# Performance work log

Measured on AMD Instinct MI355X. Metric: run time of the kernel, lower is better.

The kernel has to match this reference:

```python
import jax, jax.numpy as jnp
import numpy as np

B, INP, OUP, HID, H, W = 16, 32, 64, 192, 96, 96


def _relu6(t):
    return jnp.clip(t, 0.0, 6.0)


def _bn(t, g, b, m, v):
    # eval-mode BatchNorm2d, eps = 1e-5
    scale = g / jnp.sqrt(v + 1e-5)
    return (t - m[None, :, None, None]) * scale[None, :, None, None] + b[None, :, None, None]


def _up_bilinear_ac(img, Ho, Wo):
    # bilinear upsample with align_corners=True (torch upsample_bilinear)
    hin, win = img.shape[-2], img.shape[-1]
    def mk(nin, nout):
        c = jnp.arange(nout, dtype=jnp.float32) * ((nin - 1) / (nout - 1))
        i0 = jnp.clip(jnp.floor(c).astype(jnp.int32), 0, nin - 2)
        return i0, c - i0.astype(jnp.float32)
    r0, fr = mk(hin, Ho)
    c0, fc = mk(win, Wo)
    rows = img[..., r0, :] * (1.0 - fr)[:, None] + img[..., r0 + 1, :] * fr[:, None]
    return rows[..., c0] * (1.0 - fc) + rows[..., c0 + 1] * fc


def setup_inputs() -> dict:
    key = jax.random.key(0)
    ks = jax.random.split(key, 6)
    rn = lambda k, s, sc: jax.random.normal(k, s, dtype=jnp.float32) * sc
    return {
        'x': rn(ks[0], (B, INP, H, W), 1.0),
        'w1': rn(ks[1], (HID, INP), 0.1),
        'g1': jnp.ones((HID,), jnp.float32), 'b1': jnp.zeros((HID,), jnp.float32),
        'm1': jnp.zeros((HID,), jnp.float32), 'v1': jnp.ones((HID,), jnp.float32),
        'se_w': rn(ks[2], (1, HID), 0.1), 'se_b': jnp.zeros((1,), jnp.float32),
        'w_dw': rn(ks[3], (HID, 1, 3, 3), 0.1),
        'g2': jnp.ones((HID,), jnp.float32), 'b2': jnp.zeros((HID,), jnp.float32),
        'm2': jnp.zeros((HID,), jnp.float32), 'v2': jnp.ones((HID,), jnp.float32),
        'w2': rn(ks[4], (OUP, HID), 0.1),
        'g3': jnp.ones((OUP,), jnp.float32), 'b3': jnp.zeros((OUP,), jnp.float32),
        'm3': jnp.zeros((OUP,), jnp.float32), 'v3': jnp.ones((OUP,), jnp.float32),
    }


def reference(x, w1, g1, b1, m1, v1, se_w, se_b, w_dw, g2, b2, m2, v2, w2, g3, b3, m3, v3):
    tal = jnp.take_along_axis
    # expand 1x1 conv + BN + ReLU6
    y = jnp.einsum('bihw,oi->bohw', x, w1)
    y = _relu6(_bn(y, g1, b1, m1, v1))
    Bn, C, Hh, Ww = y.shape
    # SE branch: adaptive avg pool to 6x6 (H,W divisible by 6 -> uniform bins)
    yp = y.reshape(Bn, C, 6, Hh // 6, 6, Ww // 6).mean(axis=(3, 5))
    se = jnp.einsum('bchw,oc->bohw', yp, se_w) + se_b[None, :, None, None]
    se = jax.nn.sigmoid(se)
    se = _up_bilinear_ac(se, Hh, Ww)            # [B,1,H,W]
    y = y * se
    ys = se[:, 0]                                # [B,H,W]
    tc, tr = Ww // 2, Hh // 2
    # ---- row pass: content-adaptive sample positions via cumsum ----
    rm = ys + 0.001
    xx = jnp.cumsum((Ww * 0.5) / jnp.sum(rm, -1, keepdims=True) * rm + 0.5, axis=-1)
    xx = jax.lax.stop_gradient(xx)               # positions are detached
    cq = jnp.arange(tc, dtype=jnp.float32) * 2.0
    # searchsorted-left minus 1, clamped (torchinterp1d semantics)
    i = jnp.clip(jnp.sum(xx[..., None] < cq, axis=-2).astype(jnp.int32) - 1, 0, Ww - 2)  # [B,H,tc]
    x0 = tal(xx, i, -1); x1 = tal(xx, i + 1, -1)
    t = (cq - x0) / (x1 - x0)                    # [B,H,tc]
    ib = jnp.broadcast_to(i[:, None], (Bn, C, Hh, tc))
    y0 = tal(y, ib, -1); y1 = tal(y, ib + 1, -1)
    mf = y0 + (y1 - y0) * t[:, None]             # [B,C,H,tc]
    m0 = tal(ys, i, -1); m1_ = tal(ys, i + 1, -1)
    mm = m0 + (m1_ - m0) * t                     # [B,H,tc]
    # ---- column pass ----
    cm = mm + 0.001
    yy = jnp.cumsum((Hh * 0.5) / jnp.sum(cm, 1, keepdims=True) * cm + 0.5, axis=1)
    yy = jax.lax.stop_gradient(yy)               # [B,H,tc]
    yyT = jnp.swapaxes(yy, 1, 2)                 # [B,tc,H]
    rq = jnp.arange(tr, dtype=jnp.float32) * 2.0
    i2 = jnp.clip(jnp.sum(yyT[..., None] < rq, axis=-2).astype(jnp.int32) - 1, 0, Hh - 2)  # [B,tc,tr]
    p0 = tal(yyT, i2, -1); p1 = tal(yyT, i2 + 1, -1)
    t2 = (rq - p0) / (p1 - p0)                   # [B,tc,tr]
    mfT = jnp.swapaxes(mf, 2, 3)                 # [B,C,tc,H]
    i2b = jnp.broadcast_to(i2[:, None], (Bn, C, tc, tr))
    f0 = tal(mfT, i2b, -1); f1 = tal(mfT, i2b + 1, -1)
    ff = jnp.swapaxes(f0 + (f1 - f0) * t2[:, None], 2, 3)  # [B,C,tr,tc]
    # ---- tail: depthwise 3x3 + BN + ReLU6, project 1x1 + BN ----
    z = jax.lax.conv_general_dilated(ff, w_dw, (1, 1), 'SAME',
                                     feature_group_count=C,
                                     dimension_numbers=('NCHW', 'OIHW', 'NCHW'))
    z = _relu6(_bn(z, g2, b2, m2, v2))
    z = jnp.einsum('bchw,oc->bohw', z, w2)
    z = _bn(z, g3, b3, m3, v3)
    return z
```

## Files before the change

### kernel.cpp

```cpp
#include <hip/hip_runtime.h>
#include <hip/hip_bf16.h>
#include <math.h>

#define B_   16
#define INP  32
#define OUP  64
#define HID  192
#define H_   96
#define W_   96
#define HW_  (H_*W_)
#define TC   48
#define TR   48

typedef __attribute__((ext_vector_type(8))) short  bf16x8;
typedef __attribute__((ext_vector_type(4))) float  f32x4;

__device__ __forceinline__ float relu6f(float v) { return fminf(fmaxf(v, 0.f), 6.f); }
__device__ __forceinline__ float bf2f(unsigned short u) {
    unsigned int x = ((unsigned int)u) << 16;
    return __uint_as_float(x);
}
__device__ __forceinline__ unsigned short f2bf(float f) {
    unsigned int x = __float_as_uint(f);
    unsigned int lsb = (x >> 16) & 1u;
    x += 0x7fffu + lsb;
    return (unsigned short)(x >> 16);
}

__global__ __launch_bounds__(256) void k0_prep(
    const float* __restrict__ w1, const float* __restrict__ g1,
    const float* __restrict__ b1, const float* __restrict__ m1,
    const float* __restrict__ v1,
    const float* __restrict__ w2, const float* __restrict__ g3,
    const float* __restrict__ b3, const float* __restrict__ m3,
    const float* __restrict__ v3,
    unsigned short* __restrict__ w1b, float* __restrict__ t1,
    float* __restrict__ w2t, float* __restrict__ t3,
    float* __restrict__ se_part)
{
    const int idx = blockIdx.x*256 + threadIdx.x;
    if (idx < HID*INP) {
        int o = idx / INP;
        w1b[idx] = f2bf(w1[idx] * g1[o]*rsqrtf(v1[o] + 1e-5f));
    } else if (idx < HID*INP + HID) {
        int o = idx - HID*INP;
        float sc = g1[o]*rsqrtf(v1[o] + 1e-5f);
        t1[o] = b1[o] - m1[o]*sc;
    } else if (idx < HID*INP + HID + HID*OUP) {
        int k = idx - (HID*INP + HID);
        int c = k / OUP, o = k % OUP;
        w2t[k] = w2[o*HID + c] * g3[o]*rsqrtf(v3[o] + 1e-5f);
    } else if (idx < HID*INP + HID + HID*OUP + OUP) {
        int o = idx - (HID*INP + HID + HID*OUP);
        float sc = g3[o]*rsqrtf(v3[o] + 1e-5f);
        t3[o] = b3[o] - m3[o]*sc;
    } else if (idx < HID*INP + HID + HID*OUP + OUP + B_*36) {
        se_part[idx - (HID*INP + HID + HID*OUP + OUP)] = 0.f;
    }
}

__global__ __launch_bounds__(256) void k1_mfma(
    const float* __restrict__ x, const unsigned short* __restrict__ w1b,
    const float* __restrict__ t1, const float* __restrict__ se_w,
    unsigned short* __restrict__ y, float* __restrict__ se_part)
{
    __shared__ unsigned short wl[HID*INP];
    __shared__ unsigned short xT[64*INP];
    __shared__ float t1l[HID], sewl[HID];
    const int tid = threadIdx.x;
    const int bid = blockIdx.x;
    const int b   = bid / 144;
    const int inpx0 = (bid % 144) * 64;

    {
        const uint4* src = (const uint4*)w1b;
        uint4* dst = (uint4*)wl;
        dst[tid] = src[tid];
        if (tid < 256) { dst[tid+256] = src[tid+256]; dst[tid+512] = src[tid+512]; }
    }
    if (tid < HID) { t1l[tid] = t1[tid]; sewl[tid] = se_w[tid]; }
    {
        const int ch = tid >> 3, q8 = tid & 7;
        const float* xp = x + (size_t)(b*INP + ch)*HW_ + inpx0 + q8*8;
        float4 v0 = *(const float4*)(xp);
        float4 v1 = *(const float4*)(xp + 4);
        int p0 = q8*8;
        xT[(p0+0)*INP + ch] = f2bf(v0.x);
        xT[(p0+1)*INP + ch] = f2bf(v0.y);
        xT[(p0+2)*INP + ch] = f2bf(v0.z);
        xT[(p0+3)*INP + ch] = f2bf(v0.w);
        xT[(p0+4)*INP + ch] = f2bf(v1.x);
        xT[(p0+5)*INP + ch] = f2bf(v1.y);
        xT[(p0+6)*INP + ch] = f2bf(v1.z);
        xT[(p0+7)*INP + ch] = f2bf(v1.w);
    }
    __syncthreads();

    const int w = tid >> 6;
    const int l = tid & 63;
    const int pxl = l & 15;
    const int kb  = l >> 4;

    const bf16x8 bfrag = *(const bf16x8*)&xT[(w*16 + pxl)*INP + kb*8];

    const size_t ybase = (size_t)b*HID*HW_ + inpx0 + w*16 + pxl;
    float psum = 0.f;

    #pragma unroll
    for (int T = 0; T < 12; ++T) {
        const bf16x8 afrag = *(const bf16x8*)&wl[(T*16 + pxl)*INP + kb*8];
        f32x4 acc = __builtin_amdgcn_mfma_f32_16x16x32_bf16(
                        afrag, bfrag, (f32x4){0.f,0.f,0.f,0.f}, 0, 0, 0);
        const int oc0 = T*16 + kb*4;
        const float4 t1v = *(const float4*)&t1l[oc0];
        const float4 swv = *(const float4*)&sewl[oc0];
        float yv0 = relu6f(acc[0] + t1v.x);
        float yv1 = relu6f(acc[1] + t1v.y);
        float yv2 = relu6f(acc[2] + t1v.z);
        float yv3 = relu6f(acc[3] + t1v.w);
        psum += swv.x*yv0 + swv.y*yv1 + swv.z*yv2 + swv.w*yv3;
        y[ybase + (size_t)(oc0+0)*HW_] = f2bf(yv0);
        y[ybase + (size_t)(oc0+1)*HW_] = f2bf(yv1);
        y[ybase + (size_t)(oc0+2)*HW_] = f2bf(yv2);
        y[ybase + (size_t)(oc0+3)*HW_] = f2bf(yv3);
    }

    #pragma unroll
    for (int off = 32; off > 0; off >>= 1) psum += __shfl_down(psum, off, 64);
    if (l == 0) {
        const int spx = inpx0 + w*16;
        const int h = spx / W_, w0 = spx % W_;
        const int cell = (h >> 4)*6 + (w0 >> 4);
        atomicAdd(&se_part[b*36 + cell], psum);
    }
}

__global__ __launch_bounds__(256) void k2_se(
    const float* __restrict__ se_part, const float* __restrict__ se_b,
    float* __restrict__ se6)
{
    const int id = blockIdx.x*256 + threadIdx.x;
    if (id < B_*36) {
        float logit = se_part[id]*(1.f/256.f) + se_b[0];
        se6[id] = 1.f/(1.f + expf(-logit));
    }
}

__global__ __launch_bounds__(128) void k3_rows(
    const float* __restrict__ se6,
    int* __restrict__ iW, float* __restrict__ AW, float* __restrict__ BW,
    float* __restrict__ mm)
{
    const int bx = blockIdx.x;
    const int b = bx / H_, h = bx % H_;
    const int tid = threadIdx.x;
    __shared__ float ysr[W_];
    __shared__ float xxl[W_];

    const float* s6 = se6 + b*36;
    float ch = h * (5.0f/95.0f);
    int r0 = (int)floorf(ch); r0 = min(max(r0, 0), 4);
    float fr = ch - (float)r0;

    if (tid < W_) {
        float cw = tid * (5.0f/95.0f);
        int c0 = (int)floorf(cw); c0 = min(max(c0, 0), 4);
        float fc = cw - (float)c0;
        float v00 = s6[r0*6 + c0],     v01 = s6[r0*6 + c0 + 1];
        float v10 = s6[(r0+1)*6 + c0], v11 = s6[(r0+1)*6 + c0 + 1];
        float ra = v00*(1.f-fr) + v10*fr;
        float rb = v01*(1.f-fr) + v11*fr;
        ysr[tid] = ra*(1.f-fc) + rb*fc;
    }
    __syncthreads();
    if (tid == 0) {
        float rs = 0.f;
        for (int w = 0; w < W_; ++w) rs += ysr[w] + 0.001f;
        float scale = (W_*0.5f)/rs;
        float cum = 0.f;
        for (int w = 0; w < W_; ++w) { cum += scale*(ysr[w]+0.001f) + 0.5f; xxl[w] = cum; }
    }
    __syncthreads();
    if (tid < TC) {
        float cq = tid * 2.0f;
        int cnt = 0;
        for (int w = 0; w < W_; ++w) cnt += (xxl[w] < cq) ? 1 : 0;
        int i = min(max(cnt - 1, 0), W_ - 2);
        float x0 = xxl[i], x1 = xxl[i+1];
        float t = (cq - x0)/(x1 - x0);
        int idx = bx*TC + tid;
        float s0 = ysr[i], s1v = ysr[i+1];
        iW[idx] = i;
        AW[idx] = s0*(1.f - t);
        BW[idx] = s1v*t;
        mm[idx] = s0 + (s1v - s0)*t;
    }
}

__global__ __launch_bounds__(128) void k5_cols(
    const float* __restrict__ mm, int* __restrict__ i2T,
    float* __restrict__ A2T, float* __restrict__ B2T)
{
    const int bx = blockIdx.x;
    const int b = bx / TC, j = bx % TC;
    const int tid = threadIdx.x;
    __shared__ float cmv[H_], yyl[H_];

    if (tid < H_) cmv[tid] = mm[(b*H_ + tid)*TC + j] + 0.001f;
    __syncthreads();
    if (tid == 0) {
        float cs = 0.f;
        for (int hh = 0; hh < H_; ++hh) cs += cmv[hh];
        float scale = (H_*0.5f)/cs;
        float cum = 0.f;
        for (int hh = 0; hh < H_; ++hh) { cum += scale*cmv[hh] + 0.5f; yyl[hh] = cum; }
    }
    __syncthreads();
    if (tid < TR) {
        float rq = tid * 2.0f;
        int cnt = 0;
        for (int hh = 0; hh < H_; ++hh) cnt += (yyl[hh] < rq) ? 1 : 0;
        int i2 = min(max(cnt - 1, 0), H_ - 2);
        float p0 = yyl[i2], p1 = yyl[i2+1];
        float t2 = (rq - p0)/(p1 - p0);
        int idx = (b*TR + tid)*TC + j;
        i2T[idx] = i2; A2T[idx] = 1.f - t2; B2T[idx] = t2;
    }
}

__global__ __launch_bounds__(256) void k4_warp_dw(
    const unsigned short* __restrict__ y,
    const int* __restrict__ iW, const float* __restrict__ AW,
    const float* __restrict__ BW,
    const int* __restrict__ i2T, const float* __restrict__ A2T,
    const float* __restrict__ B2T,
    const float* __restrict__ wdw,
    const float* __restrict__ g2, const float* __restrict__ b2,
    const float* __restrict__ m2, const float* __restrict__ v2,
    float* __restrict__ z1)
{
    __shared__ unsigned short ypl[HW_];
    __shared__ float mfs[H_*TC];
    __shared__ float ffs[TR*TC];
    const int tid = threadIdx.x;
    const int b = blockIdx.x / HID;
    const int c = blockIdx.x % HID;

    const uint4* ysrc = (const uint4*)(y + (size_t)(b*HID + c)*HW_);
    uint4* ydst = (uint4*)ypl;
    for (int k = tid; k < HW_/8; k += 256) ydst[k] = ysrc[k];
    __syncthreads();

    const int rbase = b*H_*TC;
    for (int k = tid; k < H_*TC; k += 256) {
        int h = k / TC;
        int rid = rbase + k;
        int i = iW[rid];
        float y0 = bf2f(ypl[h*W_ + i]);
        float y1 = bf2f(ypl[h*W_ + i + 1]);
        mfs[k] = y0*AW[rid] + y1*BW[rid];
    }
    __syncthreads();

    const int r2base = b*TR*TC;
    for (int k = tid; k < TR*TC; k += 256) {
        int j = k % TC;
        int rid = r2base + k;
        int i2 = i2T[rid];
        ffs[k] = mfs[i2*TC + j]*A2T[rid] + mfs[(i2+1)*TC + j]*B2T[rid];
    }

    float wk[9];
    #pragma unroll
    for (int k = 0; k < 9; ++k) wk[k] = wdw[c*9 + k];
    float sc = g2[c]*rsqrtf(v2[c] + 1e-5f);
    float sh = b2[c] - m2[c]*sc;
    __syncthreads();

    float* zp = z1 + (size_t)(b*HID + c)*TR*TC;
    for (int k = tid; k < TR*TC; k += 256) {
        int r = k / TC, j = k % TC;
        float acc = 0.f;
        #pragma unroll
        for (int dr = -1; dr <= 1; ++dr)
            #pragma unroll
            for (int dj = -1; dj <= 1; ++dj) {
                int rr = r + dr, jj = j + dj;
                if (rr >= 0 && rr < TR && jj >= 0 && jj < TC)
                    acc += ffs[rr*TC + jj]*wk[(dr+1)*3 + (dj+1)];
            }
        zp[k] = relu6f(acc*sc + sh);
    }
}

__global__ __launch_bounds__(256) void k8_conv2(
    const float* __restrict__ z1, const float* __restrict__ w2t,
    const float* __restrict__ t3, float* __restrict__ out)
{
    const int tid = threadIdx.x;
    const int pxg = tid & 15;
    const int oc  = tid >> 4;
    const int pix0 = blockIdx.x*64 + pxg*4;
    const int b   = pix0 / (TR*TC);
    const int sp  = pix0 % (TR*TC);

    float acc[4][4];
    #pragma unroll
    for (int p = 0; p < 4; ++p)
        #pragma unroll
        for (int o = 0; o < 4; ++o) acc[p][o] = 0.f;

    const float* zb = z1 + (size_t)b*HID*TR*TC + sp;
    const float* wb = w2t + oc*4;
    #pragma unroll 4
    for (int c = 0; c < HID; ++c) {
        float4 z = *(const float4*)(zb + (size_t)c*TR*TC);
        float4 w = *(const float4*)(wb + c*OUP);
        acc[0][0] += z.x*w.x; acc[0][1] += z.x*w.y; acc[0][2] += z.x*w.z; acc[0][3] += z.x*w.w;
        acc[1][0] += z.y*w.x; acc[1][1] += z.y*w.y; acc[1][2] += z.y*w.z; acc[1][3] += z.y*w.w;
        acc[2][0] += z.z*w.x; acc[2][1] += z.z*w.y; acc[2][2] += z.z*w.z; acc[2][3] += z.z*w.w;
        acc[3][0] += z.w*w.x; acc[3][1] += z.w*w.y; acc[3][2] += z.w*w.z; acc[3][3] += z.w*w.w;
    }

    const float4 tt = *(const float4*)(t3 + oc*4);
    float* ob = out + (size_t)b*OUP*TR*TC + sp;
    #pragma unroll
    for (int o = 0; o < 4; ++o) {
        float tb = (o==0)?tt.x:(o==1)?tt.y:(o==2)?tt.z:tt.w;
        float4 r = make_float4(acc[0][o]+tb, acc[1][o]+tb, acc[2][o]+tb, acc[3][o]+tb);
        *(float4*)(ob + (size_t)(oc*4 + o)*TR*TC) = r;
    }
}

extern "C" void kernel_launch(void* const* d_in, const int* in_sizes, int n_in,
                              void* d_out, int out_size, void* d_ws, size_t ws_size,
                              hipStream_t stream)
{
    const float* x    = (const float*)d_in[0];
    const float* w1   = (const float*)d_in[1];
    const float* g1   = (const float*)d_in[2];
    const float* b1   = (const float*)d_in[3];
    const float* m1   = (const float*)d_in[4];
    const float* v1   = (const float*)d_in[5];
    const float* se_w = (const float*)d_in[6];
    const float* se_b = (const float*)d_in[7];
    const float* wdw  = (const float*)d_in[8];
    const float* g2   = (const float*)d_in[9];
    const float* b2   = (const float*)d_in[10];
    const float* m2   = (const float*)d_in[11];
    const float* v2   = (const float*)d_in[12];
    const float* w2   = (const float*)d_in[13];
    const float* g3   = (const float*)d_in[14];
    const float* b3   = (const float*)d_in[15];
    const float* m3   = (const float*)d_in[16];
    const float* v3   = (const float*)d_in[17];
    float* out = (float*)d_out;

    float* ws = (float*)d_ws;
    unsigned short* y = (unsigned short*)ws;
    float* z1      = ws + 14155776;
    float* se6     = ws + 21233664;
    int*   iW      = (int*)(ws + 21234240);
    float* AW      = ws + 21307968;
    float* BW      = ws + 21381696;
    float* mm      = ws + 21455424;
    int*   i2T     = (int*)(ws + 21529152);
    float* A2T     = ws + 21566016;
    float* B2T     = ws + 21602880;
    float* se_part = ws + 21639744;
    unsigned short* w1b = (unsigned short*)(ws + 21642048);
    float* t1      = ws + 21648192;
    float* w2t     = ws + 21648384;
    float* t3      = ws + 21660672;

    k0_prep<<<76, 256, 0, stream>>>(w1, g1, b1, m1, v1, w2, g3, b3, m3, v3,
                                    w1b, t1, w2t, t3, se_part);
    k1_mfma<<<B_*144, 256, 0, stream>>>(x, w1b, t1, se_w, y, se_part);
    k2_se<<<3, 256, 0, stream>>>(se_part, se_b, se6);
    k3_rows<<<B_*H_, 128, 0, stream>>>(se6, iW, AW, BW, mm);
    k5_cols<<<B_*TC, 128, 0, stream>>>(mm, i2T, A2T, B2T);
    k4_warp_dw<<<B_*HID, 256, 0, stream>>>(y, iW, AW, BW, i2T, A2T, B2T,
                                           wdw, g2, b2, m2, v2, z1);
    k8_conv2<<<(B_*TR*TC)/64, 256, 0, stream>>>(z1, w2t, t3, out);
}
```

Baseline: 215.5 us.

## Gather y directly from global in warp kernel and pack warp tables as float4

The warp/depthwise kernel no longer copies the whole bf16 channel plane into shared memory; it gathers the needed samples directly from global memory. The row and column index/weight tables are merged into float4 records so each lookup is one vector load. BN2 scale and shift are precomputed in the prep kernel, and the warp loops are fully unrolled. This reduces LDS use and redundant plane loads, at the cost of uncoalesced global gathers and larger table footprints.

```diff
diff --git a/kernel.cpp b/kernel.cpp
--- a/kernel.cpp
+++ b/kernel.cpp
@@ -34,9 +34,12 @@
     const float* __restrict__ w2, const float* __restrict__ g3,
     const float* __restrict__ b3, const float* __restrict__ m3,
     const float* __restrict__ v3,
+    const float* __restrict__ g2, const float* __restrict__ b2,
+    const float* __restrict__ m2, const float* __restrict__ v2,
     unsigned short* __restrict__ w1b, float* __restrict__ t1,
     float* __restrict__ w2t, float* __restrict__ t3,
-    float* __restrict__ se_part)
+    float* __restrict__ se_part, float* __restrict__ sc2,
+    float* __restrict__ sh2)
 {
     const int idx = blockIdx.x*256 + threadIdx.x;
     if (idx < HID*INP) {
@@ -56,6 +59,13 @@
         t3[o] = b3[o] - m3[o]*sc;
     } else if (idx < HID*INP + HID + HID*OUP + OUP + B_*36) {
         se_part[idx - (HID*INP + HID + HID*OUP + OUP)] = 0.f;
+    } else if (idx < HID*INP + HID + HID*OUP + OUP + B_*36 + HID) {
+        int c = idx - (HID*INP + HID + HID*OUP + OUP + B_*36);
+        sc2[c] = g2[c]*rsqrtf(v2[c] + 1e-5f);
+    } else if (idx < HID*INP + HID + HID*OUP + OUP + B_*36 + 2*HID) {
+        int c = idx - (HID*INP + HID + HID*OUP + OUP + B_*36 + HID);
+        float sc = g2[c]*rsqrtf(v2[c] + 1e-5f);
+        sh2[c] = b2[c] - m2[c]*sc;
     }
 }
 
@@ -102,7 +112,6 @@
     const int kb  = l >> 4;
 
     const bf16x8 bfrag = *(const bf16x8*)&xT[(w*16 + pxl)*INP + kb*8];
-
     const size_t ybase = (size_t)b*HID*HW_ + inpx0 + w*16 + pxl;
     float psum = 0.f;
 
@@ -148,8 +157,7 @@
 
 __global__ __launch_bounds__(128) void k3_rows(
     const float* __restrict__ se6,
-    int* __restrict__ iW, float* __restrict__ AW, float* __restrict__ BW,
-    float* __restrict__ mm)
+    float4* __restrict__ iABW, float* __restrict__ mm)
 {
     const int bx = blockIdx.x;
     const int b = bx / H_, h = bx % H_;
@@ -190,16 +198,13 @@
         float t = (cq - x0)/(x1 - x0);
         int idx = bx*TC + tid;
         float s0 = ysr[i], s1v = ysr[i+1];
-        iW[idx] = i;
-        AW[idx] = s0*(1.f - t);
-        BW[idx] = s1v*t;
+        iABW[idx] = make_float4((float)i, s0*(1.f - t), s1v*t, 0.f);
         mm[idx] = s0 + (s1v - s0)*t;
     }
 }
 
 __global__ __launch_bounds__(128) void k5_cols(
-    const float* __restrict__ mm, int* __restrict__ i2T,
-    float* __restrict__ A2T, float* __restrict__ B2T)
+    const float* __restrict__ mm, float4* __restrict__ i2AB)
 {
     const int bx = blockIdx.x;
     const int b = bx / TC, j = bx % TC;
@@ -224,61 +229,58 @@
         float p0 = yyl[i2], p1 = yyl[i2+1];
         float t2 = (rq - p0)/(p1 - p0);
         int idx = (b*TR + tid)*TC + j;
-        i2T[idx] = i2; A2T[idx] = 1.f - t2; B2T[idx] = t2;
+        i2AB[idx] = make_float4((float)i2, 1.f - t2, t2, 0.f);
     }
 }
 
 __global__ __launch_bounds__(256) void k4_warp_dw(
     const unsigned short* __restrict__ y,
-    const int* __restrict__ iW, const float* __restrict__ AW,
-    const float* __restrict__ BW,
-    const int* __restrict__ i2T, const float* __restrict__ A2T,
-    const float* __restrict__ B2T,
+    const float4* __restrict__ iABW,
+    const float4* __restrict__ i2AB,
     const float* __restrict__ wdw,
-    const float* __restrict__ g2, const float* __restrict__ b2,
-    const float* __restrict__ m2, const float* __restrict__ v2,
+    const float* __restrict__ sc2, const float* __restrict__ sh2,
     float* __restrict__ z1)
 {
-    __shared__ unsigned short ypl[HW_];
     __shared__ float mfs[H_*TC];
     __shared__ float ffs[TR*TC];
     const int tid = threadIdx.x;
     const int b = blockIdx.x / HID;
     const int c = blockIdx.x % HID;
-
-    const uint4* ysrc = (const uint4*)(y + (size_t)(b*HID + c)*HW_);
-    uint4* ydst = (uint4*)ypl;
-    for (int k = tid; k < HW_/8; k += 256) ydst[k] = ysrc[k];
-    __syncthreads();
+    const unsigned short* yp = y + (size_t)(b*HID + c)*HW_;
 
     const int rbase = b*H_*TC;
-    for (int k = tid; k < H_*TC; k += 256) {
+    #pragma unroll
+    for (int t = 0; t < (H_*TC)/256; ++t) {
+        int k = tid + t*256;
         int h = k / TC;
-        int rid = rbase + k;
-        int i = iW[rid];
-        float y0 = bf2f(ypl[h*W_ + i]);
-        float y1 = bf2f(ypl[h*W_ + i + 1]);
-        mfs[k] = y0*AW[rid] + y1*BW[rid];
+        float4 f = iABW[rbase + k];
+        int i = (int)f.x;
+        float y0 = bf2f(yp[h*W_ + i]);
+        float y1 = bf2f(yp[h*W_ + i + 1]);
+        mfs[k] = y0*f.y + y1*f.z;
     }
     __syncthreads();
 
     const int r2base = b*TR*TC;
-    for (int k = tid; k < TR*TC; k += 256) {
+    #pragma unroll
+    for (int t = 0; t < (TR*TC)/256; ++t) {
+        int k = tid + t*256;
         int j = k % TC;
-        int rid = r2base + k;
-        int i2 = i2T[rid];
-        ffs[k] = mfs[i2*TC + j]*A2T[rid] + mfs[(i2+1)*TC + j]*B2T[rid];
+        float4 f = i2AB[r2base + k];
+        int i2 = (int)f.x;
+        ffs[k] = mfs[i2*TC + j]*f.y + mfs[(i2+1)*TC + j]*f.z;
     }
 
     float wk[9];
     #pragma unroll
     for (int k = 0; k < 9; ++k) wk[k] = wdw[c*9 + k];
-    float sc = g2[c]*rsqrtf(v2[c] + 1e-5f);
-    float sh = b2[c] - m2[c]*sc;
+    const float sc = sc2[c], sh = sh2[c];
     __syncthreads();
 
     float* zp = z1 + (size_t)(b*HID + c)*TR*TC;
-    for (int k = tid; k < TR*TC; k += 256) {
+    #pragma unroll
+    for (int t = 0; t < (TR*TC)/256; ++t) {
+        int k = tid + t*256;
         int r = k / TC, j = k % TC;
         float acc = 0.f;
         #pragma unroll
@@ -358,28 +360,26 @@
 
     float* ws = (float*)d_ws;
     unsigned short* y = (unsigned short*)ws;
-    float* z1      = ws + 14155776;
-    float* se6     = ws + 21233664;
-    int*   iW      = (int*)(ws + 21234240);
-    float* AW      = ws + 21307968;
-    float* BW      = ws + 21381696;
-    float* mm      = ws + 21455424;
-    int*   i2T     = (int*)(ws + 21529152);
-    float* A2T     = ws + 21566016;
-    float* B2T     = ws + 21602880;
-    float* se_part = ws + 21639744;
-    unsigned short* w1b = (unsigned short*)(ws + 21642048);
-    float* t1      = ws + 21648192;
-    float* w2t     = ws + 21648384;
-    float* t3      = ws + 21660672;
-
-    k0_prep<<<76, 256, 0, stream>>>(w1, g1, b1, m1, v1, w2, g3, b3, m3, v3,
-                                    w1b, t1, w2t, t3, se_part);
+    float*  z1     = ws + 14155776;
+    float*  se6    = ws + 21233664;
+    float4* iABW   = (float4*)(ws + 21234240);
+    float*  mm     = ws + 21529152;
+    float4* i2AB   = (float4*)(ws + 21602880);
+    float*  se_part= ws + 21750336;
+    unsigned short* w1b = (unsigned short*)(ws + 21750912);
+    float*  t1     = ws + 21753984;
+    float*  w2t    = ws + 21754176;
+    float*  t3     = ws + 21766464;
+    float*  sc2    = ws + 21766528;
+    float*  sh2    = ws + 21766720;
+
+    k0_prep<<<77, 256, 0, stream>>>(w1, g1, b1, m1, v1, w2, g3, b3, m3, v3,
+                                    g2, b2, m2, v2,
+                                    w1b, t1, w2t, t3, se_part, sc2, sh2);
     k1_mfma<<<B_*144, 256, 0, stream>>>(x, w1b, t1, se_w, y, se_part);
     k2_se<<<3, 256, 0, stream>>>(se_part, se_b, se6);
-    k3_rows<<<B_*H_, 128, 0, stream>>>(se6, iW, AW, BW, mm);
-    k5_cols<<<B_*TC, 128, 0, stream>>>(mm, i2T, A2T, B2T);
-    k4_warp_dw<<<B_*HID, 256, 0, stream>>>(y, iW, AW, BW, i2T, A2T, B2T,
-                                           wdw, g2, b2, m2, v2, z1);
+    k3_rows<<<B_*H_, 128, 0, stream>>>(se6, iABW, mm);
+    k5_cols<<<B_*TC, 128, 0, stream>>>(mm, i2AB);
+    k4_warp_dw<<<B_*HID, 256, 0, stream>>>(y, iABW, i2AB, wdw, sc2, sh2, z1);
     k8_conv2<<<(B_*TR*TC)/64, 256, 0, stream>>>(z1, w2t, t3, out);
 }
```

After: 190.6 us. 1.13x faster.
